# Optimization experiments

Hardware: AMD Instinct MI355X
Metric: run time of the kernel (lower is better)

The kernel has to match this reference:

```python
import jax, jax.numpy as jnp
import numpy as np

KSIZE = 7
PAD = KSIZE // 2          # reflection pad radius
EPS_BN = 1e-5             # CONFIG.model.arch.batchnorm_eps
SCALE = 1.0               # self.scale
BN_W, BN_B = 0.1, 0.0     # BatchNorm init per module


def _l2n(x, eps=1e-12):
    return x / (jnp.linalg.norm(x) + eps)


def setup_inputs() -> dict:
    key = jax.random.key(0)
    ks = jax.random.split(key, 6)
    B, Cg, Co, H, W = 2, 128, 32, 512, 512
    f = jax.random.normal(ks[0], (B, Cg, H, W), jnp.float32)
    alpha = jax.random.normal(ks[1], (B, Co, H, W), jnp.float32)
    # guidance_conv: 1x1 conv Cg -> Cg//2 (xavier-ish init)
    wg = jax.random.normal(ks[2], (Cg // 2, Cg), jnp.float32) * (1.0 / np.sqrt(Cg))
    bg = jnp.zeros((Cg // 2,), jnp.float32)
    # spectral-norm 1x1 conv Co -> Co, no bias
    w_bar = jax.random.normal(ks[3], (Co, Co), jnp.float32) * (1.0 / np.sqrt(Co))
    u = _l2n(jax.random.normal(ks[4], (Co,), jnp.float32))
    v = _l2n(jax.random.normal(ks[5], (Co,), jnp.float32))
    return {"f": f, "alpha": alpha, "wg": wg, "bg": bg, "w_bar": w_bar, "u": u, "v": v}


def reference(f, alpha, wg, bg, w_bar, u, v):
    B, _, H, W = f.shape
    # 1x1 guidance conv
    g = jnp.einsum('oc,bchw->bohw', wg, f) + bg[None, :, None, None]
    # hop_normalize: channel-wise L2 normalize, clamped at 1e-4
    gn = g / jnp.maximum(jnp.linalg.norm(g, axis=1, keepdims=True), 1e-4)
    r = jnp.pad(gn, ((0, 0), (0, 0), (PAD, PAD), (PAD, PAD)), mode='reflect')
    # ksize^2 shifted-window correlation -> scores [K2, B, 1, H, W]
    scores = []
    for i in range(KSIZE):
        for j in range(KSIZE):
            if i == PAD and j == PAD:
                scores.append(jnp.full((B, 1, H, W), -10000.0, gn.dtype))
            else:
                scores.append((gn * r[:, :, i:i + H, j:j + W]).sum(axis=1, keepdims=True))
    s = jax.nn.softmax(jnp.stack(scores, axis=0) * SCALE, axis=0)
    # weighted neighborhood aggregation of alpha (skip center tap)
    alp = jnp.pad(alpha, ((0, 0), (0, 0), (PAD, PAD), (PAD, PAD)), mode='reflect')
    y = jnp.zeros_like(alpha)
    for i in range(KSIZE):
        for j in range(KSIZE):
            if i == PAD and j == PAD:
                continue
            y = y + alp[:, :, i:i + H, j:j + W] * s[i * KSIZE + j]
    # spectral-norm 1x1 conv (training: one detached power iteration)
    v1 = jax.lax.stop_gradient(_l2n(w_bar.T @ u))
    u1 = jax.lax.stop_gradient(_l2n(w_bar @ v1))
    sigma = u1 @ (w_bar @ v1)
    w_sn = w_bar / sigma
    y2 = jnp.einsum('oc,bchw->bohw', w_sn, y)
    # BatchNorm2d, training mode (batch stats), weight=0.1 bias=0
    mean = y2.mean(axis=(0, 2, 3), keepdims=True)
    var = y2.var(axis=(0, 2, 3), keepdims=True)
    y_bn = BN_W * (y2 - mean) / jnp.sqrt(var + EPS_BN) + BN_B
    return y_bn + alpha
```

## Files before the change

### kernel.cpp

```cpp
#include <hip/hip_runtime.h>

#define HWc   262144
#define CGc   128
#define CHc   64
#define COc   32
#define NPIXc 524288
#define TW 32
#define TH 8
#define HLW 38
#define HLH 14
#define HPX (HLW*HLH)

typedef _Float16 h2    __attribute__((ext_vector_type(2)));
typedef __fp16   fp2   __attribute__((ext_vector_type(2)));
typedef _Float16 f16x8 __attribute__((ext_vector_type(8)));
typedef float    f32x4 __attribute__((ext_vector_type(4)));

union AB { uint4 q; f16x8 v; h2 p[4]; unsigned u[4]; };

__device__ __forceinline__ int refl(int p){
  if (p < 0) p = -p;
  else if (p >= 512) p = 1022 - p;
  return p;
}
__device__ __forceinline__ h2 as_h2(unsigned u){ union{unsigned u; h2 h;} x; x.u = u; return x.h; }
__device__ __forceinline__ unsigned as_u(h2 h){ union{unsigned u; h2 h;} x; x.h = h; return x.u; }
__device__ __forceinline__ unsigned pkh(float a, float b){
  h2 h; h.x = (_Float16)a; h.y = (_Float16)b; return as_u(h);
}
__device__ __forceinline__ h2 pkrtz(float a, float b){
  union{ fp2 f; h2 h; } x; x.f = __builtin_amdgcn_cvt_pkrtz(a, b); return x.h;
}
__device__ __forceinline__ float2 upk(unsigned u){
  h2 h = as_h2(u); return make_float2((float)h.x, (float)h.y);
}
__device__ __forceinline__ float dot2h(unsigned a, unsigned b, float c){
  return __builtin_amdgcn_fdot2(as_h2(a), as_h2(b), c, false);
}
__device__ __forceinline__ unsigned pkfma16(unsigned a, unsigned b, unsigned c){
  unsigned d;
  asm("v_pk_fma_f16 %0, %1, %2, %3" : "=v"(d) : "v"(a), "v"(b), "v"(c));
  return d;
}
__device__ __forceinline__ f32x4 mfma32(f16x8 a, f16x8 b, f32x4 c){
  return __builtin_amdgcn_mfma_f32_16x16x32_f16(a, b, c, 0, 0, 0);
}

__global__ void k0_prep(const float* __restrict__ wbar, const float* __restrict__ u,
                        const float* __restrict__ wg,
                        unsigned* __restrict__ wgA, unsigned* __restrict__ wsnA){
  const int t = threadIdx.x;
  __shared__ float sv1[32];
  float tv = 0.f;
  if (t < 32){
    #pragma unroll
    for (int o = 0; o < 32; o++) tv += wbar[o*32 + t] * u[o];
  }
  float sq = tv * tv;
  #pragma unroll
  for (int off = 32; off; off >>= 1) sq += __shfl_down(sq, off);
  const float n1 = sqrtf(__shfl(sq, 0)) + 1e-12f;
  if (t < 32) sv1[t] = tv / n1;
  __syncthreads();
  float tu = 0.f;
  if (t < 32){
    #pragma unroll
    for (int c = 0; c < 32; c++) tu += wbar[t*32 + c] * sv1[c];
  }
  float sq2 = tu * tu;
  #pragma unroll
  for (int off = 32; off; off >>= 1) sq2 += __shfl_down(sq2, off);
  const float S = __shfl(sq2, 0);
  const float inv = (sqrtf(S) + 1e-12f) / S;

  for (int k = t; k < 4096; k += 64){
    const int mk = k >> 8, L = (k >> 2) & 63, j = k & 3;
    const int m = mk >> 2, ks = mk & 3;
    const int o = m*16 + (L & 15);
    const int c = ks*32 + 8*(L >> 4) + 2*j;
    wgA[k] = pkh(wg[o*128 + c], wg[o*128 + c + 1]);
  }
  for (int k = t; k < 512; k += 64){
    const int m = k >> 8, L = (k >> 2) & 63, j = k & 3;
    const int o = m*16 + (L & 15);
    const int c = 8*(L >> 4) + 2*j;
    wsnA[k] = pkh(wbar[o*32 + c] * inv, wbar[o*32 + c + 1] * inv);
  }
}

__global__ __launch_bounds__(256) void k1m(const float* __restrict__ f,
                                           const float* __restrict__ alpha,
                                           const uint4* __restrict__ wgA,
                                           const uint4* __restrict__ wsnA,
                                           const float* __restrict__ bg,
                                           unsigned* __restrict__ gn,
                                           unsigned* __restrict__ apm){
  const int tid  = threadIdx.x;
  const int lane = tid & 63, w = tid >> 6;
  const int lo   = lane & 15, hi = lane >> 4;

  AB wga[4][4];
  #pragma unroll
  for (int m = 0; m < 4; m++)
    #pragma unroll
    for (int ks = 0; ks < 4; ks++)
      wga[m][ks].q = wgA[(m*4 + ks)*64 + lane];
  AB wsa[2];
  #pragma unroll
  for (int m = 0; m < 2; m++) wsa[m].q = wsnA[m*64 + lane];
  float4 bgl[4];
  #pragma unroll
  for (int m = 0; m < 4; m++) bgl[m] = *(const float4*)(bg + m*16 + hi*4);

  const int pxg = blockIdx.x * 256 + w * 64;

  auto loadT = [&](int nt, float* fv, float* av){
    const int px0  = pxg + nt*16;
    const int b    = px0 >> 18;
    const int pix0 = px0 & (HWc - 1);
    const float* fb = f + (size_t)b * CGc * HWc + pix0 + lo;
    const float* ac = alpha + (size_t)b * COc * HWc + pix0 + lo + (size_t)(hi*8) * HWc;
    #pragma unroll
    for (int ks = 0; ks < 4; ks++){
      const float* fc = fb + (size_t)(ks*32 + hi*8) * HWc;
      #pragma unroll
      for (int e = 0; e < 8; e++)
        fv[ks*8 + e] = fc[(size_t)e * HWc];
    }
    #pragma unroll
    for (int e = 0; e < 8; e++)
      av[e] = ac[(size_t)e * HWc];
  };

  auto procT = [&](int nt, const float* fv, const float* av){
    const int px0  = pxg + nt*16;

    f32x4 acc[4];
    #pragma unroll
    for (int m = 0; m < 4; m++) acc[m] = (f32x4){0.f, 0.f, 0.f, 0.f};

    #pragma unroll
    for (int ks = 0; ks < 4; ks++){
      AB bf;
      #pragma unroll
      for (int j = 0; j < 4; j++)
        bf.p[j] = pkrtz(fv[ks*8 + 2*j], fv[ks*8 + 2*j + 1]);
      #pragma unroll
      for (int m = 0; m < 4; m++)
        acc[m] = mfma32(wga[m][ks].v, bf.v, acc[m]);
    }

    float v[16]; float nsq = 0.f;
    #pragma unroll
    for (int m = 0; m < 4; m++){
      v[4*m+0] = acc[m][0] + bgl[m].x;
      v[4*m+1] = acc[m][1] + bgl[m].y;
      v[4*m+2] = acc[m][2] + bgl[m].z;
      v[4*m+3] = acc[m][3] + bgl[m].w;
      nsq = fmaf(v[4*m+0], v[4*m+0], nsq); nsq = fmaf(v[4*m+1], v[4*m+1], nsq);
      nsq = fmaf(v[4*m+2], v[4*m+2], nsq); nsq = fmaf(v[4*m+3], v[4*m+3], nsq);
    }
    nsq += __shfl_xor(nsq, 16);
    nsq += __shfl_xor(nsq, 32);
    const float inv = 1.f / fmaxf(sqrtf(nsq), 1e-4f);

    unsigned* gp = gn + (size_t)(px0 + lo) * 32 + hi*2;
    #pragma unroll
    for (int m = 0; m < 4; m++){
      uint2 st = make_uint2(pkh(v[4*m+0]*inv, v[4*m+1]*inv),
                            pkh(v[4*m+2]*inv, v[4*m+3]*inv));
      *(uint2*)(gp + m*8) = st;
    }

    AB af;
    #pragma unroll
    for (int j = 0; j < 4; j++)
      af.p[j] = pkrtz(av[2*j], av[2*j + 1]);
    unsigned* op = apm + (size_t)(px0 + lo) * 16 + hi*2;
    #pragma unroll
    for (int m = 0; m < 2; m++){
      f32x4 aa = (f32x4){0.f, 0.f, 0.f, 0.f};
      aa = mfma32(wsa[m].v, af.v, aa);
      uint2 st = make_uint2(pkh(aa[0], aa[1]), pkh(aa[2], aa[3]));
      *(uint2*)(op + m*8) = st;
    }
  };

  float fv0[32], av0[8], fv1[32], av1[8];
  loadT(0, fv0, av0);
  loadT(1, fv1, av1);
  procT(0, fv0, av0);
  loadT(2, fv0, av0);
  procT(1, fv1, av1);
  loadT(3, fv1, av1);
  procT(2, fv0, av0);
  procT(3, fv1, av1);
}

__global__ __launch_bounds__(256) void k2_agg(const unsigned* __restrict__ gn,
                                              const unsigned* __restrict__ apm,
                                              unsigned* __restrict__ y2){
  __shared__ uint4 gs4[8][HPX];

  const int lb  = (blockIdx.x & 7) * 256 + (blockIdx.x >> 3);
  const int txx = lb & 15;
  const int tyy = (lb >> 4) & 63;
  const int bb  = lb >> 10;
  const int x0  = txx * TW, y0 = tyy * TH;
  const int tid = threadIdx.x;

  for (int t = tid; t < HPX; t += 256){
    const int hr = t / HLW;
    const int hc = t - hr * HLW;
    const int gy = refl(y0 + hr - 3);
    const int gx = refl(x0 + hc - 3);
    const uint4* src = (const uint4*)(gn + (size_t)((bb << 18) + (gy << 9) + gx) * 32);
    #pragma unroll
    for (int k = 0; k < 8; k++) gs4[k][t] = src[k];
  }
  __syncthreads();

  const int r  = tid >> 5, c = tid & 31;
  const int yy = y0 + r,  xx = x0 + c;
  const int self = (r + 3) * HLW + (c + 3);

  uint4 cv[8];
  #pragma unroll
  for (int k = 0; k < 8; k++) cv[k] = gs4[k][self];

  int ax[7];
  #pragma unroll
  for (int j = 0; j < 7; j++) ax[j] = refl(xx + j - 3);

  unsigned ya[16];
  #pragma unroll
  for (int k = 0; k < 16; k++) ya[k] = 0u;
  float esum = 0.f;

  #pragma unroll 1
  for (int i = 0; i < 7; i++){
    const int ay = refl(yy + i - 3);
    const unsigned* aprow = apm + (size_t)((bb << 18) + (ay << 9)) * 16;
    const int rowbase = (r + i) * HLW + c;
    #pragma unroll
    for (int j = 0; j < 7; j++){
      if (i == 3 && j == 3) continue;
      const int hp = rowbase + j;
      float s0 = 0.f, s1 = 0.f, s2 = 0.f, s3 = 0.f;
      #pragma unroll
      for (int k = 0; k < 8; k++){
        const uint4 q = gs4[k][hp];
        s0 = dot2h(cv[k].x, q.x, s0);
        s1 = dot2h(cv[k].y, q.y, s1);
        s2 = dot2h(cv[k].z, q.z, s2);
        s3 = dot2h(cv[k].w, q.w, s3);
      }
      const float e = __expf((s0 + s1) + (s2 + s3));
      esum += e;
      const unsigned eh = as_u(pkrtz(e, e));
      const uint4* ap = (const uint4*)(aprow + (size_t)ax[j] * 16);
      #pragma unroll
      for (int kk = 0; kk < 4; kk++){
        const uint4 a = ap[kk];
        ya[4*kk+0] = pkfma16(a.x, eh, ya[4*kk+0]);
        ya[4*kk+1] = pkfma16(a.y, eh, ya[4*kk+1]);
        ya[4*kk+2] = pkfma16(a.z, eh, ya[4*kk+2]);
        ya[4*kk+3] = pkfma16(a.w, eh, ya[4*kk+3]);
      }
    }
  }

  const float inv = 1.f / esum;
  unsigned yw[16];
  #pragma unroll
  for (int k = 0; k < 16; k++){
    const float2 t2 = upk(ya[k]);
    yw[k] = pkh(t2.x * inv, t2.y * inv);
  }
  uint4* yp = (uint4*)(y2 + (size_t)((bb << 18) + (yy << 9) + xx) * 16);
  #pragma unroll
  for (int k = 0; k < 4; k++)
    yp[k] = make_uint4(yw[4*k], yw[4*k+1], yw[4*k+2], yw[4*k+3]);
}

__global__ __launch_bounds__(256) void k3_stats(const unsigned* __restrict__ y2,
                                                float* __restrict__ stats){
  float s[COc], q[COc];
  #pragma unroll
  for (int o = 0; o < COc; o++){ s[o] = 0.f; q[o] = 0.f; }
  const int stride = gridDim.x * 256;
  for (int p = blockIdx.x * 256 + threadIdx.x; p < NPIXc; p += stride){
    const uint4* yp = (const uint4*)(y2 + (size_t)p * 16);
    #pragma unroll
    for (int k = 0; k < 4; k++){
      const uint4 w = yp[k];
      const unsigned vv[4] = {w.x, w.y, w.z, w.w};
      #pragma unroll
      for (int m = 0; m < 4; m++){
        const float2 ab = upk(vv[m]);
        s[8*k+2*m]   += ab.x; q[8*k+2*m]   = fmaf(ab.x, ab.x, q[8*k+2*m]);
        s[8*k+2*m+1] += ab.y; q[8*k+2*m+1] = fmaf(ab.y, ab.y, q[8*k+2*m+1]);
      }
    }
  }
  #pragma unroll
  for (int o = 0; o < COc; o++){
    #pragma unroll
    for (int off = 32; off; off >>= 1){
      s[o] += __shfl_down(s[o], off);
      q[o] += __shfl_down(q[o], off);
    }
  }
  __shared__ float red[4][64];
  const int wv = threadIdx.x >> 6;
  if ((threadIdx.x & 63) == 0){
    #pragma unroll
    for (int o = 0; o < COc; o++){ red[wv][o] = s[o]; red[wv][32 + o] = q[o]; }
  }
  __syncthreads();
  if (threadIdx.x < 64){
    const float v = red[0][threadIdx.x] + red[1][threadIdx.x]
                  + red[2][threadIdx.x] + red[3][threadIdx.x];
    atomicAdd(&stats[threadIdx.x], v);
  }
}

__global__ void k3b_final(const float* __restrict__ stats, float* __restrict__ stats2){
  const int t = threadIdx.x;
  if (t < COc){
    const float invN = 1.f / (float)NPIXc;
    const float mean = stats[t] * invN;
    const float var  = fmaf(-mean, mean, stats[COc + t] * invN);
    stats2[t]       = mean;
    stats2[COc + t] = 0.1f * rsqrtf(var + 1e-5f);
  }
}

__global__ __launch_bounds__(256) void k4_out(const unsigned* __restrict__ y2,
                                              const float* __restrict__ alpha,
                                              const float* __restrict__ stats2,
                                              float* __restrict__ out){
  const int p   = blockIdx.x * 256 + threadIdx.x;
  const int b   = p >> 18;
  const int pix = p & (HWc - 1);
  const uint4* yp = (const uint4*)(y2 + (size_t)p * 16);
  const size_t boff = (size_t)b * COc * HWc + pix;
  #pragma unroll
  for (int k = 0; k < 4; k++){
    const uint4 w = yp[k];
    const unsigned vv[4] = {w.x, w.y, w.z, w.w};
    #pragma unroll
    for (int m = 0; m < 4; m++){
      const int o = 8*k + 2*m;
      const float2 ab = upk(vv[m]);
      out[boff + (size_t)o*HWc]     = fmaf(ab.x - stats2[o],   stats2[COc+o],
                                           alpha[boff + (size_t)o*HWc]);
      out[boff + (size_t)(o+1)*HWc] = fmaf(ab.y - stats2[o+1], stats2[COc+o+1],
                                           alpha[boff + (size_t)(o+1)*HWc]);
    }
  }
}

extern "C" void kernel_launch(void* const* d_in, const int* in_sizes, int n_in,
                              void* d_out, int out_size, void* d_ws, size_t ws_size,
                              hipStream_t stream){
  const float* f     = (const float*)d_in[0];
  const float* alpha = (const float*)d_in[1];
  const float* wg    = (const float*)d_in[2];
  const float* bg    = (const float*)d_in[3];
  const float* wbar  = (const float*)d_in[4];
  const float* u     = (const float*)d_in[5];
  (void)in_sizes; (void)n_in; (void)out_size; (void)ws_size;
  float* out = (float*)d_out;

  char* ws = (char*)d_ws;
  float*    stats  = (float*)ws;
  float*    stats2 = (float*)(ws + 4096);
  unsigned* wgA    = (unsigned*)(ws + 8192);
  unsigned* wsnA   = (unsigned*)(ws + 32768);
  unsigned* apm    = (unsigned*)(ws + 65536);
  unsigned* gn     = (unsigned*)(ws + 65536 + (size_t)NPIXc*64);
  unsigned* y2     = (unsigned*)(ws + 65536 + (size_t)NPIXc*64 + (size_t)NPIXc*128);

  (void)hipMemsetAsync(stats, 0, 64 * sizeof(float), stream);
  k0_prep  <<<1, 64, 0, stream>>>(wbar, u, wg, wgA, wsnA);
  k1m      <<<NPIXc / 256, 256, 0, stream>>>(f, alpha, (const uint4*)wgA,
                                             (const uint4*)wsnA, bg, gn, apm);
  k2_agg   <<<2048, 256, 0, stream>>>(gn, apm, y2);
  k3_stats <<<256, 256, 0, stream>>>(y2, stats);
  k3b_final<<<1, 64, 0, stream>>>(stats, stats2);
  k4_out   <<<NPIXc / 256, 256, 0, stream>>>(y2, alpha, stats2, out);
}
```

Measured before the change: 309.0 us.

## Stage guidance and alpha inputs through LDS with 128-pixel coalesced loads

```diff
diff --git a/kernel.cpp b/kernel.cpp
--- a/kernel.cpp
+++ b/kernel.cpp
@@ -10,6 +10,7 @@
 #define HLW 38
 #define HLH 14
 #define HPX (HLW*HLH)
+#define FLS 132
 
 typedef _Float16 h2    __attribute__((ext_vector_type(2)));
 typedef __fp16   fp2   __attribute__((ext_vector_type(2)));
@@ -95,9 +96,13 @@
                                            const float* __restrict__ bg,
                                            unsigned* __restrict__ gn,
                                            unsigned* __restrict__ apm){
+  __shared__ unsigned ldsf[64 * FLS];
+  __shared__ unsigned ldsa[16 * FLS];
+
   const int tid  = threadIdx.x;
   const int lane = tid & 63, w = tid >> 6;
   const int lo   = lane & 15, hi = lane >> 4;
+  const int tpx  = tid & 127, th = tid >> 7;
 
   AB wga[4][4];
   #pragma unroll
@@ -112,89 +117,87 @@
   #pragma unroll
   for (int m = 0; m < 4; m++) bgl[m] = *(const float4*)(bg + m*16 + hi*4);
 
-  const int pxg = blockIdx.x * 256 + w * 64;
-
-  auto loadT = [&](int nt, float* fv, float* av){
-    const int px0  = pxg + nt*16;
-    const int b    = px0 >> 18;
-    const int pix0 = px0 & (HWc - 1);
-    const float* fb = f + (size_t)b * CGc * HWc + pix0 + lo;
-    const float* ac = alpha + (size_t)b * COc * HWc + pix0 + lo + (size_t)(hi*8) * HWc;
-    #pragma unroll
-    for (int ks = 0; ks < 4; ks++){
-      const float* fc = fb + (size_t)(ks*32 + hi*8) * HWc;
-      #pragma unroll
-      for (int e = 0; e < 8; e++)
-        fv[ks*8 + e] = fc[(size_t)e * HWc];
-    }
-    #pragma unroll
-    for (int e = 0; e < 8; e++)
-      av[e] = ac[(size_t)e * HWc];
-  };
-
-  auto procT = [&](int nt, const float* fv, const float* av){
-    const int px0  = pxg + nt*16;
-
-    f32x4 acc[4];
-    #pragma unroll
-    for (int m = 0; m < 4; m++) acc[m] = (f32x4){0.f, 0.f, 0.f, 0.f};
-
-    #pragma unroll
-    for (int ks = 0; ks < 4; ks++){
-      AB bf;
+  const int px0  = blockIdx.x * 256;
+  const int b    = px0 >> 18;
+  const int pix0 = px0 & (HWc - 1);
+
+  #pragma unroll 1
+  for (int half = 0; half < 2; half++){
+    const int pbase = pix0 + half*128;
+    const float* fb = f + (size_t)b * CGc * HWc + pbase + tpx;
+    const float* ab = alpha + (size_t)b * COc * HWc + pbase + tpx;
+
+    #pragma unroll
+    for (int i = 0; i < 32; i++){
+      const int cp = th + 2*i;
+      ldsf[cp*FLS + tpx] = as_u(pkrtz(fb[(size_t)(2*cp) * HWc],
+                                      fb[(size_t)(2*cp + 1) * HWc]));
+    }
+    #pragma unroll
+    for (int i = 0; i < 8; i++){
+      const int cp = th + 2*i;
+      ldsa[cp*FLS + tpx] = as_u(pkrtz(ab[(size_t)(2*cp) * HWc],
+                                      ab[(size_t)(2*cp + 1) * HWc]));
+    }
+    __syncthreads();
+
+    #pragma unroll
+    for (int ntl = 0; ntl < 2; ntl++){
+      const int pxl = w*32 + ntl*16 + lo;
+      const int pxg = px0 + half*128 + w*32 + ntl*16;
+
+      f32x4 acc[4];
+      #pragma unroll
+      for (int m = 0; m < 4; m++) acc[m] = (f32x4){0.f, 0.f, 0.f, 0.f};
+
+      #pragma unroll
+      for (int ks = 0; ks < 4; ks++){
+        AB bf;
+        #pragma unroll
+        for (int j = 0; j < 4; j++)
+          bf.u[j] = ldsf[(ks*16 + hi*4 + j)*FLS + pxl];
+        #pragma unroll
+        for (int m = 0; m < 4; m++)
+          acc[m] = mfma32(wga[m][ks].v, bf.v, acc[m]);
+      }
+
+      float v[16]; float nsq = 0.f;
+      #pragma unroll
+      for (int m = 0; m < 4; m++){
+        v[4*m+0] = acc[m][0] + bgl[m].x;
+        v[4*m+1] = acc[m][1] + bgl[m].y;
+        v[4*m+2] = acc[m][2] + bgl[m].z;
+        v[4*m+3] = acc[m][3] + bgl[m].w;
+        nsq = fmaf(v[4*m+0], v[4*m+0], nsq); nsq = fmaf(v[4*m+1], v[4*m+1], nsq);
+        nsq = fmaf(v[4*m+2], v[4*m+2], nsq); nsq = fmaf(v[4*m+3], v[4*m+3], nsq);
+      }
+      nsq += __shfl_xor(nsq, 16);
+      nsq += __shfl_xor(nsq, 32);
+      const float inv = 1.f / fmaxf(sqrtf(nsq), 1e-4f);
+
+      unsigned* gp = gn + (size_t)(pxg + lo) * 32 + hi*2;
+      #pragma unroll
+      for (int m = 0; m < 4; m++){
+        uint2 st = make_uint2(pkh(v[4*m+0]*inv, v[4*m+1]*inv),
+                              pkh(v[4*m+2]*inv, v[4*m+3]*inv));
+        *(uint2*)(gp + m*8) = st;
+      }
+
+      AB af;
       #pragma unroll
       for (int j = 0; j < 4; j++)
-        bf.p[j] = pkrtz(fv[ks*8 + 2*j], fv[ks*8 + 2*j + 1]);
-      #pragma unroll
-      for (int m = 0; m < 4; m++)
-        acc[m] = mfma32(wga[m][ks].v, bf.v, acc[m]);
-    }
-
-    float v[16]; float nsq = 0.f;
-    #pragma unroll
-    for (int m = 0; m < 4; m++){
-      v[4*m+0] = acc[m][0] + bgl[m].x;
-      v[4*m+1] = acc[m][1] + bgl[m].y;
-      v[4*m+2] = acc[m][2] + bgl[m].z;
-      v[4*m+3] = acc[m][3] + bgl[m].w;
-      nsq = fmaf(v[4*m+0], v[4*m+0], nsq); nsq = fmaf(v[4*m+1], v[4*m+1], nsq);
-      nsq = fmaf(v[4*m+2], v[4*m+2], nsq); nsq = fmaf(v[4*m+3], v[4*m+3], nsq);
-    }
-    nsq += __shfl_xor(nsq, 16);
-    nsq += __shfl_xor(nsq, 32);
-    const float inv = 1.f / fmaxf(sqrtf(nsq), 1e-4f);
-
-    unsigned* gp = gn + (size_t)(px0 + lo) * 32 + hi*2;
-    #pragma unroll
-    for (int m = 0; m < 4; m++){
-      uint2 st = make_uint2(pkh(v[4*m+0]*inv, v[4*m+1]*inv),
-                            pkh(v[4*m+2]*inv, v[4*m+3]*inv));
-      *(uint2*)(gp + m*8) = st;
-    }
-
-    AB af;
-    #pragma unroll
-    for (int j = 0; j < 4; j++)
-      af.p[j] = pkrtz(av[2*j], av[2*j + 1]);
-    unsigned* op = apm + (size_t)(px0 + lo) * 16 + hi*2;
-    #pragma unroll
-    for (int m = 0; m < 2; m++){
-      f32x4 aa = (f32x4){0.f, 0.f, 0.f, 0.f};
-      aa = mfma32(wsa[m].v, af.v, aa);
-      uint2 st = make_uint2(pkh(aa[0], aa[1]), pkh(aa[2], aa[3]));
-      *(uint2*)(op + m*8) = st;
-    }
-  };
-
-  float fv0[32], av0[8], fv1[32], av1[8];
-  loadT(0, fv0, av0);
-  loadT(1, fv1, av1);
-  procT(0, fv0, av0);
-  loadT(2, fv0, av0);
-  procT(1, fv1, av1);
-  loadT(3, fv1, av1);
-  procT(2, fv0, av0);
-  procT(3, fv1, av1);
+        af.u[j] = ldsa[(hi*4 + j)*FLS + pxl];
+      unsigned* op = apm + (size_t)(pxg + lo) * 16 + hi*2;
+      #pragma unroll
+      for (int m = 0; m < 2; m++){
+        f32x4 aa = (f32x4){0.f, 0.f, 0.f, 0.f};
+        aa = mfma32(wsa[m].v, af.v, aa);
+        uint2 st = make_uint2(pkh(aa[0], aa[1]), pkh(aa[2], aa[3]));
+        *(uint2*)(op + m*8) = st;
+      }
+    }
+    __syncthreads();
+  }
 }
 
 __global__ __launch_bounds__(256) void k2_agg(const unsigned* __restrict__ gn,
```

Result: slower. 402.6 us (+30.3%).
